# Kernel optimization log

Measured on AMD Instinct MI355X. Metric: run time of the kernel, lower is better.

The kernel has to match this reference:

```python
import jax, jax.numpy as jnp
import numpy as np
from functools import partial

MAX_INSTANCES = 8


def _conv(x, W, b):
    y = jax.lax.conv_general_dilated(x, W, (1, 1), 'SAME',
                                     dimension_numbers=('NHWC', 'HWIO', 'NHWC'))
    return jax.nn.relu(y + b)


def _conv_stack(x, params):
    for W, b in params:
        x = _conv(x, W, b)
    return x


def _resize_and_pad(feat, info, bg_h, bg_w):
    # feat: (h, w, c); info: [y1, y2, x1, x2] fractions of bg size.
    # Bilinear resize (half-pixel centers, like tf.image.resize) of feat to
    # (y_size, x_size), then zero-pad into the (bg_h, bg_w) canvas at
    # (y_front, x_front). Expressed as a fixed-shape gather + validity mask
    # so it is jit-compatible despite data-dependent box sizes.
    h, w, _ = feat.shape
    y_size = jnp.maximum((bg_h * (info[1] - info[0])).astype(jnp.int32), 1)
    x_size = jnp.maximum((bg_w * (info[3] - info[2])).astype(jnp.int32), 1)
    y_front = (bg_h * info[0]).astype(jnp.int32)
    x_front = (bg_w * info[2]).astype(jnp.int32)

    def axis(bg_n, front, size, n_in):
        loc = jnp.arange(bg_n) - front
        valid = (loc >= 0) & (loc < size)
        src = (loc.astype(jnp.float32) + 0.5) * (n_in / size.astype(jnp.float32)) - 0.5
        src = jnp.clip(src, 0.0, n_in - 1.0)
        i0 = jnp.floor(src).astype(jnp.int32)
        i1 = jnp.minimum(i0 + 1, n_in - 1)
        return i0, i1, src - i0.astype(jnp.float32), valid

    y0, y1i, fy, vy = axis(bg_h, y_front, y_size, h)
    x0, x1i, fx, vx = axis(bg_w, x_front, x_size, w)
    g = lambda yi, xi: feat[yi][:, xi]  # (bg_h, bg_w, c)
    fy = fy[:, None, None]
    fx = fx[None, :, None]
    out = (g(y0, x0) * (1 - fy) * (1 - fx) + g(y0, x1i) * (1 - fy) * fx
           + g(y1i, x0) * fy * (1 - fx) + g(y1i, x1i) * fy * fx)
    return out * (vy[:, None] & vx[None, :]).astype(feat.dtype)[:, :, None]


def setup_inputs() -> dict:
    key = jax.random.key(0)
    ks = jax.random.split(key, 16)
    B, H, W, C = 4, 128, 128, 64
    h = w = 64
    hm = wm = 56
    U = 64
    MI = MAX_INSTANCES
    instance_feature = jax.random.normal(ks[0], (B, h, w, C, MI), jnp.float32)
    bg_feature = jax.random.normal(ks[1], (B, H, W, C), jnp.float32)
    # Valid boxes: 0 <= y1 < y2 <= 1, 0 <= x1 < x2 <= 1, layout (B, 4, MI).
    y1 = jax.random.uniform(ks[2], (B, 1, MI), minval=0.0, maxval=0.45)
    hh = jax.random.uniform(ks[3], (B, 1, MI), minval=0.2, maxval=0.5)
    x1 = jax.random.uniform(ks[4], (B, 1, MI), minval=0.0, maxval=0.45)
    ww = jax.random.uniform(ks[5], (B, 1, MI), minval=0.2, maxval=0.5)
    bbox = jnp.concatenate([y1, y1 + hh, x1, x1 + ww], axis=1)
    mrcnn_mask = jax.random.uniform(ks[6], (B, hm, wm, MI), jnp.float32)
    s = 0.05  # small weights keep exp() of relu conv outputs well-scaled
    return {
        'instance_feature': instance_feature,
        'bg_feature': bg_feature,
        'bbox': bbox,
        'mrcnn_mask': mrcnn_mask,
        'iW1': jax.random.normal(ks[7], (3, 3, C, U), jnp.float32) * s,
        'ib1': jnp.zeros((U,), jnp.float32),
        'iW2': jax.random.normal(ks[8], (3, 3, U, U), jnp.float32) * s,
        'ib2': jnp.zeros((U,), jnp.float32),
        'iW3': jax.random.normal(ks[9], (3, 3, U, 1), jnp.float32) * s,
        'ib3': jnp.zeros((1,), jnp.float32),
        'bW1': jax.random.normal(ks[10], (3, 3, C, U), jnp.float32) * s,
        'bb1': jnp.zeros((U,), jnp.float32),
        'bW2': jax.random.normal(ks[11], (3, 3, U, U), jnp.float32) * s,
        'bb2': jnp.zeros((U,), jnp.float32),
        'bW3': jax.random.normal(ks[12], (3, 3, U, 1), jnp.float32) * s,
        'bb3': jnp.zeros((1,), jnp.float32),
    }


def reference(instance_feature, bg_feature, bbox, mrcnn_mask,
              iW1, ib1, iW2, ib2, iW3, ib3,
              bW1, bb1, bW2, bb2, bW3, bb3):
    B, H, W, C = bg_feature.shape
    MI = instance_feature.shape[-1]
    h, w = instance_feature.shape[1], instance_feature.shape[2]
    # pack_instance -> conv stack -> unpack (kept as (B, MI, h, w, 1))
    packed = jnp.transpose(instance_feature, (0, 4, 1, 2, 3)).reshape(B * MI, h, w, C)
    iw = _conv_stack(packed, [(iW1, ib1), (iW2, ib2), (iW3, ib3)]).reshape(B, MI, h, w, 1)
    bgw = _conv_stack(bg_feature, [(bW1, bb1), (bW2, bb2), (bW3, bb3)])  # (B,H,W,1)

    rp = jax.vmap(jax.vmap(partial(_resize_and_pad, bg_h=H, bg_w=W)))
    bbox_t = jnp.transpose(bbox, (0, 2, 1))  # (B, MI, 4)
    rw = rp(iw, bbox_t)  # (B, MI, H, W, 1)
    full = jnp.broadcast_to(jnp.array([0.0, 1.0, 0.0, 1.0], jnp.float32), (B, MI, 4))
    rm = rp(jnp.moveaxis(mrcnn_mask, -1, 1)[..., None], full)  # (B, MI, H, W, 1)
    rsf = rp(jnp.moveaxis(instance_feature, -1, 1), bbox_t)  # (B, MI, H, W, C)

    ew = jnp.exp(rw) * rm          # per-instance exp weight, masked
    ew_bg = jnp.exp(bgw)           # (B, H, W, 1)
    denom = ew.sum(axis=1) + ew_bg  # (B, H, W, 1)
    return (ew_bg / denom) * bg_feature + jnp.sum(rsf * (ew / denom[:, None]), axis=1)
```

## Files before the change

### kernel.cpp

```cpp
#include <hip/hip_runtime.h>
#include <cstdint>

typedef short bf16x8 __attribute__((ext_vector_type(8)));
typedef float f32x4 __attribute__((ext_vector_type(4)));
typedef unsigned short u16;
typedef unsigned short u16x8 __attribute__((ext_vector_type(8)));
typedef unsigned int u32;

__device__ inline u16 f2bf(float f) {
  union { float f; unsigned u; } x; x.f = f;
  unsigned u = x.u + 0x7fffu + ((x.u >> 16) & 1u);
  return (u16)(u >> 16);
}
__device__ inline float bf2f(u16 h) {
  union { unsigned u; float f; } x; x.u = ((unsigned)h) << 16;
  return x.f;
}

__global__ __launch_bounds__(256) void prep_kernel(
    const float* __restrict__ inst, u16* __restrict__ pf,
    const float* __restrict__ w0, const float* __restrict__ w1,
    const float* __restrict__ w2, const float* __restrict__ w3,
    u16* __restrict__ wtr,
    const float* __restrict__ bgf, u16* __restrict__ bgp, int nT)
{
  if ((int)blockIdx.x < nT) {
    const int lane = threadIdx.x & 63;
    const int wvid = blockIdx.x * 4 + (threadIdx.x >> 6);
    const int b = wvid >> 12;
    const int pix = wvid & 4095;
    const float* s = inst + ((size_t)(b * 4096 + pix)) * 512 + lane * 8;
    float4 v0 = *(const float4*)s;
    float4 v1 = *(const float4*)(s + 4);
    float vals[8] = {v0.x, v0.y, v0.z, v0.w, v1.x, v1.y, v1.z, v1.w};
    #pragma unroll
    for (int i = 0; i < 8; i++)
      pf[(((size_t)(b * 8 + i)) * 4096 + pix) * 64 + lane] = f2bf(vals[i]);
  } else if ((int)blockIdx.x < nT + 576) {
    int id = (blockIdx.x - nT) * 256 + threadIdx.x;
    if (id >= 147456) return;
    int s = id / 36864;
    int r = id - s * 36864;
    int tap = r >> 12;
    int rc = r & 4095;
    int c = rc >> 6, u = rc & 63;
    const float* Ws = (s == 0) ? w0 : (s == 1) ? w1 : (s == 2) ? w2 : w3;
    wtr[(size_t)s * 36864 + ((size_t)tap * 64 + u) * 64 + c] =
        f2bf(Ws[((size_t)tap * 64 + c) * 64 + u]);
  } else {
    size_t id = (size_t)(blockIdx.x - nT - 576) * 256 + threadIdx.x;
    const float* s = bgf + id * 8;
    float4 v0 = *(const float4*)s;
    float4 v1 = *(const float4*)(s + 4);
    u16x8 o;
    o[0] = f2bf(v0.x); o[1] = f2bf(v0.y); o[2] = f2bf(v0.z); o[3] = f2bf(v0.w);
    o[4] = f2bf(v1.x); o[5] = f2bf(v1.y); o[6] = f2bf(v1.z); o[7] = f2bf(v1.w);
    *(u16x8*)(bgp + id * 8) = o;
  }
}

#define BOFF 41472
template<int SRC>
__device__ __forceinline__ void conv_body(
    char* smem, const void* __restrict__ inv, const u16* __restrict__ wtr,
    const float* __restrict__ bias, u16* __restrict__ out,
    int H, int W, int bid)
{
  const int tilesX = W >> 4;
  const int tilesPerImg = (H >> 4) * tilesX;
  const int img = bid / tilesPerImg;
  const int tile = bid - img * tilesPerImg;
  const int ty = (tile / tilesX) << 4;
  const int tx = (tile % tilesX) << 4;
  const int tid = threadIdx.x;

  for (int idx = tid; idx < 2592; idx += 256) {
    int hpix = idx >> 3;
    int c0 = (idx & 7) << 3;
    int hy = hpix / 18, hx = hpix - hy * 18;
    int gy = ty + hy - 1, gx = tx + hx - 1;
    u16x8 v = {0, 0, 0, 0, 0, 0, 0, 0};
    if (gy >= 0 && gy < H && gx >= 0 && gx < W) {
      if (SRC == 0) {
        const float* s = (const float*)inv + ((size_t)img * H * W + (size_t)gy * W + gx) * 64 + c0;
        #pragma unroll
        for (int j = 0; j < 8; j++) v[j] = f2bf(s[j]);
      } else if (SRC == 1) {
        const u16* s = (const u16*)inv + ((size_t)img * H * W + (size_t)gy * W + gx) * 64 + c0;
        v = *(const u16x8*)s;
      } else {
        int bb = img >> 3, ii = img & 7;
        const float* s = (const float*)inv + ((((size_t)bb * 64 + gy) * 64 + gx) * 64 + c0) * 8 + ii;
        #pragma unroll
        for (int j = 0; j < 8; j++) v[j] = f2bf(s[j * 8]);
      }
    }
    int byte = (hpix * 128 + c0 * 2) ^ ((hpix & 7) << 4);
    *(u16x8*)(smem + byte) = v;
  }

  const int lane = tid & 63;
  const int wv = tid >> 6;
  const int lrow = lane & 15;
  const int kg = lane >> 4;

  const int ch0 = tid, ch1 = tid + 256;
  const int bu0 = ch0 >> 3, bc0 = (ch0 & 7) << 3;
  const int bu1 = ch1 >> 3, bc1 = (ch1 & 7) << 3;
  const int bdst0 = BOFF + ((bu0 * 128 + bc0 * 2) ^ ((bu0 & 7) << 4));
  const int bdst1 = BOFF + ((bu1 * 128 + bc1 * 2) ^ ((bu1 & 7) << 4));

  {
    u16x8 n0 = *(const u16x8*)(wtr + (size_t)(0 * 64 + bu0) * 64 + bc0);
    u16x8 n1 = *(const u16x8*)(wtr + (size_t)(0 * 64 + bu1) * 64 + bc1);
    *(u16x8*)(smem + bdst0) = n0;
    *(u16x8*)(smem + bdst1) = n1;
  }
  __syncthreads();

  int pyv[4], pxv[4];
  #pragma unroll
  for (int mf = 0; mf < 4; mf++) {
    int p = wv * 64 + mf * 16 + lrow;
    pyv[mf] = p >> 4; pxv[mf] = p & 15;
  }

  f32x4 acc[4][4];
  #pragma unroll
  for (int a = 0; a < 4; a++)
    #pragma unroll
    for (int b = 0; b < 4; b++) { f32x4 z = {0.f, 0.f, 0.f, 0.f}; acc[a][b] = z; }

  for (int tap = 0; tap < 9; tap++) {
    u16x8 n0, n1;
    if (tap < 8) {
      n0 = *(const u16x8*)(wtr + (size_t)((tap + 1) * 64 + bu0) * 64 + bc0);
      n1 = *(const u16x8*)(wtr + (size_t)((tap + 1) * 64 + bu1) * 64 + bc1);
    }
    const int ky = tap / 3, kx = tap - ky * 3;
    #pragma unroll
    for (int ks = 0; ks < 2; ks++) {
      bf16x8 Bf[4];
      #pragma unroll
      for (int nf = 0; nf < 4; nf++) {
        int u = nf * 16 + lrow;
        int byte = BOFF + ((u * 128 + ks * 64 + kg * 16) ^ ((u & 7) << 4));
        Bf[nf] = *(const bf16x8*)(smem + byte);
      }
      #pragma unroll
      for (int mf = 0; mf < 4; mf++) {
        int hpix = (pyv[mf] + ky) * 18 + pxv[mf] + kx;
        int byte = (hpix * 128 + ks * 64 + kg * 16) ^ ((hpix & 7) << 4);
        bf16x8 Af = *(const bf16x8*)(smem + byte);
        #pragma unroll
        for (int nf = 0; nf < 4; nf++)
          acc[mf][nf] = __builtin_amdgcn_mfma_f32_16x16x32_bf16(Af, Bf[nf], acc[mf][nf], 0, 0, 0);
      }
    }
    __syncthreads();
    if (tap < 8) {
      *(u16x8*)(smem + bdst0) = n0;
      *(u16x8*)(smem + bdst1) = n1;
      __syncthreads();
    }
  }

  float bv[4];
  #pragma unroll
  for (int nf = 0; nf < 4; nf++) bv[nf] = bias[nf * 16 + lrow];

  const size_t obase = (size_t)img * H * W;
  #pragma unroll
  for (int mf = 0; mf < 4; mf++) {
    #pragma unroll
    for (int j = 0; j < 4; j++) {
      int p = wv * 64 + mf * 16 + kg * 4 + j;
      int oy = ty + (p >> 4), ox = tx + (p & 15);
      u16* op = out + (obase + (size_t)oy * W + ox) * 64 + lrow;
      #pragma unroll
      for (int nf = 0; nf < 4; nf++)
        op[nf * 16] = f2bf(fmaxf(acc[mf][nf][j] + bv[nf], 0.0f));
    }
  }
}

template<int S1, int S2>
__global__ __launch_bounds__(256) void conv_dual(
    const void* in1, const u16* w1, const float* b1, u16* o1, int H1, int W1, int split,
    const void* in2, const u16* w2, const float* b2, u16* o2, int H2, int W2)
{
  extern __shared__ float4 smem_f4[];
  char* smem = (char*)smem_f4;
  if ((int)blockIdx.x < split)
    conv_body<S1>(smem, in1, w1, b1, o1, H1, W1, blockIdx.x);
  else
    conv_body<S2>(smem, in2, w2, b2, o2, H2, W2, blockIdx.x - split);
}

__device__ __forceinline__ void conv3_body(
    char* smem, const u16* __restrict__ in, const float* __restrict__ W3,
    const float* __restrict__ b3, float* __restrict__ out, int H, int W, int bid)
{
  float* wlds = (float*)(smem + 41472);
  const int tilesX = W >> 4;
  const int tilesPerImg = (H >> 4) * tilesX;
  const int img = bid / tilesPerImg;
  const int tile = bid - img * tilesPerImg;
  const int ty = (tile / tilesX) << 4;
  const int tx = (tile % tilesX) << 4;
  const int tid = threadIdx.x;

  for (int idx = tid; idx < 2592; idx += 256) {
    int hpix = idx >> 3;
    int c0 = (idx & 7) << 3;
    int hy = hpix / 18, hx = hpix - hy * 18;
    int gy = ty + hy - 1, gx = tx + hx - 1;
    u16x8 v = {0, 0, 0, 0, 0, 0, 0, 0};
    if (gy >= 0 && gy < H && gx >= 0 && gx < W)
      v = *(const u16x8*)(in + ((size_t)img * H * W + (size_t)gy * W + gx) * 64 + c0);
    int byte = (hpix * 128 + c0 * 2) ^ ((hpix & 7) << 4);
    *(u16x8*)(smem + byte) = v;
  }
  for (int idx = tid; idx < 576; idx += 256) wlds[idx] = W3[idx];
  __syncthreads();

  const int py = tid >> 4, px = tid & 15;
  float acc = 0.0f;
  #pragma unroll
  for (int ky = 0; ky < 3; ky++) {
    #pragma unroll
    for (int kx = 0; kx < 3; kx++) {
      const int hpix = (py + ky) * 18 + (px + kx);
      const float* wp = wlds + (ky * 3 + kx) * 64;
      #pragma unroll
      for (int cg = 0; cg < 8; cg++) {
        int byte = (hpix * 128 + cg * 16) ^ ((hpix & 7) << 4);
        u16x8 v = *(const u16x8*)(smem + byte);
        #pragma unroll
        for (int j = 0; j < 8; j++)
          acc = fmaf(bf2f(v[j]), wp[cg * 8 + j], acc);
      }
    }
  }
  out[(size_t)img * H * W + (size_t)(ty + py) * W + (tx + px)] =
      fmaxf(acc + b3[0], 0.0f);
}

__global__ __launch_bounds__(256) void conv3_dual(
    const u16* in1, const float* W31, const float* b31, float* o1, int H1, int W1, int split,
    const u16* in2, const float* W32, const float* b32, float* o2, int H2, int W2)
{
  extern __shared__ float4 smem_f4[];
  char* smem = (char*)smem_f4;
  if ((int)blockIdx.x < split)
    conv3_body(smem, in1, W31, b31, o1, H1, W1, blockIdx.x);
  else
    conv3_body(smem, in2, W32, b32, o2, H2, W2, blockIdx.x - split);
}

__global__ __launch_bounds__(256) void precompute_params(
    const float* __restrict__ bbox, const float* __restrict__ mask,
    const float* __restrict__ iw, const float* __restrict__ bgw,
    float* __restrict__ pp_wbg, float4* __restrict__ pp_s)
{
  const int gpix = blockIdx.x * 256 + threadIdx.x;
  const int b = gpix >> 14;
  const int p = gpix & 16383;
  const int Y = p >> 7, X = p & 127;

  float msy = ((float)Y + 0.5f) * 0.4375f - 0.5f;
  msy = fminf(fmaxf(msy, 0.0f), 55.0f);
  int my0 = (int)floorf(msy); int my1 = min(my0 + 1, 55); float fmy = msy - (float)my0;
  float msx = ((float)X + 0.5f) * 0.4375f - 0.5f;
  msx = fminf(fmaxf(msx, 0.0f), 55.0f);
  int mx0 = (int)floorf(msx); int mx1 = min(mx0 + 1, 55); float fmx = msx - (float)mx0;

  const float ewbg = expf(bgw[gpix]);
  float denom = ewbg;
  float wi_l[8];
  u32 yx_l[8];
  float fy_l[8], fx_l[8];

  #pragma unroll
  for (int i = 0; i < 8; i++) {
    float by1 = bbox[(b * 4 + 0) * 8 + i];
    float by2 = bbox[(b * 4 + 1) * 8 + i];
    float bx1 = bbox[(b * 4 + 2) * 8 + i];
    float bx2 = bbox[(b * 4 + 3) * 8 + i];
    int ysz = max((int)(128.0f * (by2 - by1)), 1);
    int xsz = max((int)(128.0f * (bx2 - bx1)), 1);
    int yfr = (int)(128.0f * by1);
    int xfr = (int)(128.0f * bx1);
    int ly = Y - yfr, lx = X - xfr;
    bool valid = (ly >= 0) && (ly < ysz) && (lx >= 0) && (lx < xsz);
    float rwv = 0.0f;
    int y0 = 0, y1i = 0, x0 = 0, x1i = 0;
    float fy = 0.0f, fx = 0.0f;
    if (valid) {
      float sy = ((float)ly + 0.5f) * (64.0f / (float)ysz) - 0.5f;
      sy = fminf(fmaxf(sy, 0.0f), 63.0f);
      y0 = (int)floorf(sy); y1i = min(y0 + 1, 63); fy = sy - (float)y0;
      float sx = ((float)lx + 0.5f) * (64.0f / (float)xsz) - 0.5f;
      sx = fminf(fmaxf(sx, 0.0f), 63.0f);
      x0 = (int)floorf(sx); x1i = min(x0 + 1, 63); fx = sx - (float)x0;
      const float* iwp = iw + ((size_t)(b * 8 + i)) * 4096;
      float v00 = iwp[y0 * 64 + x0],  v01 = iwp[y0 * 64 + x1i];
      float v10 = iwp[y1i * 64 + x0], v11 = iwp[y1i * 64 + x1i];
      rwv = v00 * (1.f - fy) * (1.f - fx) + v01 * (1.f - fy) * fx
          + v10 * fy * (1.f - fx)         + v11 * fy * fx;
    }
    const float* mp = mask + (size_t)b * 56 * 56 * 8 + i;
    float m00 = mp[(my0 * 56 + mx0) * 8], m01 = mp[(my0 * 56 + mx1) * 8];
    float m10 = mp[(my1 * 56 + mx0) * 8], m11 = mp[(my1 * 56 + mx1) * 8];
    float rm = m00 * (1.f - fmy) * (1.f - fmx) + m01 * (1.f - fmy) * fmx
             + m10 * fmy * (1.f - fmx)         + m11 * fmy * fmx;
    float ew = expf(rwv) * rm;
    denom += ew;
    wi_l[i] = valid ? ew : 0.0f;
    yx_l[i] = (u32)y0 | ((u32)x0 << 8) | ((u32)y1i << 16) | ((u32)x1i << 24);
    fy_l[i] = fy; fx_l[i] = fx;
  }

  const float invd = 1.0f / denom;
  pp_wbg[gpix] = ewbg * invd;
  float4* qs = pp_s + ((size_t)gpix << 3);
  #pragma unroll
  for (int i = 0; i < 8; i++) {
    float4 q;
    q.x = wi_l[i] * invd;
    q.y = fy_l[i];
    q.z = fx_l[i];
    q.w = __uint_as_float(yx_l[i]);
    qs[i] = q;
  }
}

__global__ __launch_bounds__(256) void final_blend(
    const u16* __restrict__ pf, const float* __restrict__ bgf,
    const float* __restrict__ pp_wbg, const float4* __restrict__ pp_s,
    float* __restrict__ out)
{
  const int lane = threadIdx.x & 63;
  const int gpix = blockIdx.x * 4 + (threadIdx.x >> 6);
  const int b = gpix >> 14;

  float4 q[8];
  const float4* qs = pp_s + ((size_t)gpix << 3);
  #pragma unroll
  for (int i = 0; i < 8; i++) q[i] = qs[i];

  float accv = pp_wbg[gpix] * bgf[(size_t)gpix * 64 + lane];
  const u16* pfb = pf + (size_t)b * 8 * 262144;
  #pragma unroll
  for (int i = 0; i < 8; i++) {
    if (q[i].x != 0.0f) {
      u32 yx = __float_as_uint(q[i].w);
      int y0 = yx & 255, x0 = (yx >> 8) & 255;
      int y1i = (yx >> 16) & 255, x1i = (yx >> 24) & 255;
      const u16* fp = pfb + (size_t)i * 262144;
      float g00 = bf2f(fp[((size_t)(y0 * 64 + x0)) * 64 + lane]);
      float g01 = bf2f(fp[((size_t)(y0 * 64 + x1i)) * 64 + lane]);
      float g10 = bf2f(fp[((size_t)(y1i * 64 + x0)) * 64 + lane]);
      float g11 = bf2f(fp[((size_t)(y1i * 64 + x1i)) * 64 + lane]);
      float s = g00 * (1.f - q[i].y) * (1.f - q[i].z) + g01 * (1.f - q[i].y) * q[i].z
              + g10 * q[i].y * (1.f - q[i].z)         + g11 * q[i].y * q[i].z;
      accv = fmaf(q[i].x, s, accv);
    }
  }
  out[(size_t)gpix * 64 + lane] = accv;
}

__global__ __launch_bounds__(256) void final_kernel_fb(
    const float* __restrict__ inst, const float* __restrict__ bgf,
    const float* __restrict__ bbox, const float* __restrict__ mask,
    const float* __restrict__ iw, const float* __restrict__ bgw,
    float* __restrict__ out)
{
  const int lane = threadIdx.x & 63;
  const int wvid = blockIdx.x * 4 + (threadIdx.x >> 6);
  const int nw = gridDim.x * 4;
  for (int pix = wvid; pix < 4 * 128 * 128; pix += nw) {
    const int b = pix >> 14;
    const int p = pix & 16383;
    const int Y = p >> 7, X = p & 127;

    float msy = ((float)Y + 0.5f) * 0.4375f - 0.5f;
    msy = fminf(fmaxf(msy, 0.0f), 55.0f);
    int my0 = (int)floorf(msy); int my1 = min(my0 + 1, 55); float fmy = msy - (float)my0;
    float msx = ((float)X + 0.5f) * 0.4375f - 0.5f;
    msx = fminf(fmaxf(msx, 0.0f), 55.0f);
    int mx0 = (int)floorf(msx); int mx1 = min(mx0 + 1, 55); float fmx = msx - (float)mx0;

    const float ewbg = expf(bgw[(size_t)b * 16384 + p]);
    float denom = ewbg;
    float acc = 0.0f;

    for (int i = 0; i < 8; i++) {
      float by1 = bbox[(b * 4 + 0) * 8 + i];
      float by2 = bbox[(b * 4 + 1) * 8 + i];
      float bx1 = bbox[(b * 4 + 2) * 8 + i];
      float bx2 = bbox[(b * 4 + 3) * 8 + i];
      int ysz = max((int)(128.0f * (by2 - by1)), 1);
      int xsz = max((int)(128.0f * (bx2 - bx1)), 1);
      int yfr = (int)(128.0f * by1);
      int xfr = (int)(128.0f * bx1);
      int ly = Y - yfr, lx = X - xfr;
      bool valid = (ly >= 0) && (ly < ysz) && (lx >= 0) && (lx < xsz);
      float rwv = 0.0f;
      int y0 = 0, y1i = 0, x0 = 0, x1i = 0;
      float fy = 0.0f, fx = 0.0f;
      if (valid) {
        float sy = ((float)ly + 0.5f) * (64.0f / (float)ysz) - 0.5f;
        sy = fminf(fmaxf(sy, 0.0f), 63.0f);
        y0 = (int)floorf(sy); y1i = min(y0 + 1, 63); fy = sy - (float)y0;
        float sx = ((float)lx + 0.5f) * (64.0f / (float)xsz) - 0.5f;
        sx = fminf(fmaxf(sx, 0.0f), 63.0f);
        x0 = (int)floorf(sx); x1i = min(x0 + 1, 63); fx = sx - (float)x0;
        const float* iwp = iw + ((size_t)(b * 8 + i)) * 4096;
        float v00 = iwp[y0 * 64 + x0],  v01 = iwp[y0 * 64 + x1i];
        float v10 = iwp[y1i * 64 + x0], v11 = iwp[y1i * 64 + x1i];
        rwv = v00 * (1.f - fy) * (1.f - fx) + v01 * (1.f - fy) * fx
            + v10 * fy * (1.f - fx)         + v11 * fy * fx;
      }
      const float* mp = mask + (size_t)b * 56 * 56 * 8 + i;
      float m00 = mp[(my0 * 56 + mx0) * 8], m01 = mp[(my0 * 56 + mx1) * 8];
      float m10 = mp[(my1 * 56 + mx0) * 8], m11 = mp[(my1 * 56 + mx1) * 8];
      float rm = m00 * (1.f - fmy) * (1.f - fmx) + m01 * (1.f - fmy) * fmx
               + m10 * fmy * (1.f - fmx)         + m11 * fmy * fmx;
      float ew = expf(rwv) * rm;
      denom += ew;
      if (valid) {
        const float* fp = inst + (size_t)b * 2097152 + i;
        float g00 = fp[(((size_t)y0 * 64 + x0) * 64 + lane) * 8];
        float g01 = fp[(((size_t)y0 * 64 + x1i) * 64 + lane) * 8];
        float g10 = fp[(((size_t)y1i * 64 + x0) * 64 + lane) * 8];
        float g11 = fp[(((size_t)y1i * 64 + x1i) * 64 + lane) * 8];
        float s = g00 * (1.f - fy) * (1.f - fx) + g01 * (1.f - fy) * fx
                + g10 * fy * (1.f - fx)         + g11 * fy * fx;
        acc += ew * s;
      }
    }
    const float bgv = bgf[((size_t)b * 16384 + p) * 64 + lane];
    out[((size_t)b * 16384 + p) * 64 + lane] = (ewbg * bgv + acc) / denom;
  }
}

extern "C" void kernel_launch(void* const* d_in, const int* in_sizes, int n_in,
                              void* d_out, int out_size, void* d_ws, size_t ws_size,
                              hipStream_t stream) {
  const float* inst = (const float*)d_in[0];
  const float* bgf  = (const float*)d_in[1];
  const float* bbox = (const float*)d_in[2];
  const float* mask = (const float*)d_in[3];
  const float* iW1 = (const float*)d_in[4];  const float* ib1 = (const float*)d_in[5];
  const float* iW2 = (const float*)d_in[6];  const float* ib2 = (const float*)d_in[7];
  const float* iW3 = (const float*)d_in[8];  const float* ib3 = (const float*)d_in[9];
  const float* bW1 = (const float*)d_in[10]; const float* bb1 = (const float*)d_in[11];
  const float* bW2 = (const float*)d_in[12]; const float* bb2 = (const float*)d_in[13];
  const float* bW3 = (const float*)d_in[14]; const float* bb3 = (const float*)d_in[15];

  char* ws = (char*)d_ws;
  u16*   wtr  = (u16*)ws;
  u16*   AbI  = (u16*)(ws + 294912);
  u16*   AbB  = (u16*)(ws + 17072128);
  u16*   BbI  = (u16*)(ws + 25460736);
  u16*   BbB  = (u16*)(ws + 42237952);
  float* iw   = (float*)(ws + 50626560);
  float* bgw  = (float*)(ws + 51150848);
  u16*   pf   = (u16*)(ws + 51412992);
  u16*   bgp  = (u16*)(ws + 68190208);
  const bool usePf = ws_size >= (size_t)76578816;
  float* outp = (float*)d_out;

  float*  pp_wbg = (float*) (ws + 294912);
  float4* pp_s   = (float4*)(ws + 294912 + 262144);

  if (usePf) {
    prep_kernel<<<6720, 256, 0, stream>>>(inst, pf, iW1, iW2, bW1, bW2, wtr,
                                          bgf, bgp, 4096);
    conv_dual<1, 1><<<768, 256, 49664, stream>>>(
        pf,  wtr,             ib1, AbI, 64, 64, 512,
        bgp, wtr + 2 * 36864, bb1, AbB, 128, 128);
    conv_dual<1, 1><<<768, 256, 49664, stream>>>(
        AbI, wtr + 36864,     ib2, BbI, 64, 64, 512,
        AbB, wtr + 3 * 36864, bb2, BbB, 128, 128);
    conv3_dual<<<768, 256, 43776, stream>>>(
        BbI, iW3, ib3, iw, 64, 64, 512,
        BbB, bW3, bb3, bgw, 128, 128);
    precompute_params<<<256, 256, 0, stream>>>(bbox, mask, iw, bgw, pp_wbg, pp_s);
    final_blend<<<16384, 256, 0, stream>>>(pf, bgf, pp_wbg, pp_s, outp);
  } else {
    prep_kernel<<<576, 256, 0, stream>>>(inst, pf, iW1, iW2, bW1, bW2, wtr,
                                         bgf, bgp, 0);
    conv_dual<2, 0><<<768, 256, 49664, stream>>>(
        inst, wtr,            ib1, AbI, 64, 64, 512,
        bgf, wtr + 2 * 36864, bb1, AbB, 128, 128);
    conv_dual<1, 1><<<768, 256, 49664, stream>>>(
        AbI, wtr + 36864,     ib2, BbI, 64, 64, 512,
        AbB, wtr + 3 * 36864, bb2, BbB, 128, 128);
    conv3_dual<<<768, 256, 43776, stream>>>(
        BbI, iW3, ib3, iw, 64, 64, 512,
        BbB, bW3, bb3, bgw, 128, 128);
    final_kernel_fb<<<2048, 256, 0, stream>>>(inst, bgf, bbox, mask, iw, bgw, outp);
  }
}
```

Before: 115.1 us.

## Enlarge conv tiles to 32x16 and double-buffer weight slices in LDS

The 3x3 conv kernels now process 32x16 output tiles per block, with 8 M-fragments per wave, so the halo overhead per output and the number of blocks both shrink. Weight tap slices are double-buffered in LDS, which removes one __syncthreads per tap. Shared memory is now statically sized (about 93KB), and launch bounds are set to one block per CU. The cost is fewer blocks (384) and higher register pressure from 32 accumulators per lane, which may reduce occupancy and latency hiding.

```diff
diff --git a/kernel.cpp b/kernel.cpp
--- a/kernel.cpp
+++ b/kernel.cpp
@@ -59,7 +59,7 @@
   }
 }
 
-#define BOFF 41472
+#define BOFF0 78336
 template<int SRC>
 __device__ __forceinline__ void conv_body(
     char* smem, const void* __restrict__ inv, const u16* __restrict__ wtr,
@@ -67,14 +67,14 @@
     int H, int W, int bid)
 {
   const int tilesX = W >> 4;
-  const int tilesPerImg = (H >> 4) * tilesX;
+  const int tilesPerImg = (H >> 5) * tilesX;
   const int img = bid / tilesPerImg;
   const int tile = bid - img * tilesPerImg;
-  const int ty = (tile / tilesX) << 4;
+  const int ty = (tile / tilesX) << 5;
   const int tx = (tile % tilesX) << 4;
   const int tid = threadIdx.x;
 
-  for (int idx = tid; idx < 2592; idx += 256) {
+  for (int idx = tid; idx < 4896; idx += 256) {
     int hpix = idx >> 3;
     int c0 = (idx & 7) << 3;
     int hy = hpix / 18, hx = hpix - hy * 18;
@@ -107,27 +107,27 @@
   const int ch0 = tid, ch1 = tid + 256;
   const int bu0 = ch0 >> 3, bc0 = (ch0 & 7) << 3;
   const int bu1 = ch1 >> 3, bc1 = (ch1 & 7) << 3;
-  const int bdst0 = BOFF + ((bu0 * 128 + bc0 * 2) ^ ((bu0 & 7) << 4));
-  const int bdst1 = BOFF + ((bu1 * 128 + bc1 * 2) ^ ((bu1 & 7) << 4));
+  const int brel0 = (bu0 * 128 + bc0 * 2) ^ ((bu0 & 7) << 4);
+  const int brel1 = (bu1 * 128 + bc1 * 2) ^ ((bu1 & 7) << 4);
 
   {
-    u16x8 n0 = *(const u16x8*)(wtr + (size_t)(0 * 64 + bu0) * 64 + bc0);
-    u16x8 n1 = *(const u16x8*)(wtr + (size_t)(0 * 64 + bu1) * 64 + bc1);
-    *(u16x8*)(smem + bdst0) = n0;
-    *(u16x8*)(smem + bdst1) = n1;
+    u16x8 n0 = *(const u16x8*)(wtr + (size_t)bu0 * 64 + bc0);
+    u16x8 n1 = *(const u16x8*)(wtr + (size_t)bu1 * 64 + bc1);
+    *(u16x8*)(smem + BOFF0 + brel0) = n0;
+    *(u16x8*)(smem + BOFF0 + brel1) = n1;
   }
   __syncthreads();
 
-  int pyv[4], pxv[4];
-  #pragma unroll
-  for (int mf = 0; mf < 4; mf++) {
-    int p = wv * 64 + mf * 16 + lrow;
+  int pyv[8], pxv[8];
+  #pragma unroll
+  for (int mf = 0; mf < 8; mf++) {
+    int p = wv * 128 + mf * 16 + lrow;
     pyv[mf] = p >> 4; pxv[mf] = p & 15;
   }
 
-  f32x4 acc[4][4];
-  #pragma unroll
-  for (int a = 0; a < 4; a++)
+  f32x4 acc[8][4];
+  #pragma unroll
+  for (int a = 0; a < 8; a++)
     #pragma unroll
     for (int b = 0; b < 4; b++) { f32x4 z = {0.f, 0.f, 0.f, 0.f}; acc[a][b] = z; }
 
@@ -138,17 +138,18 @@
       n1 = *(const u16x8*)(wtr + (size_t)((tap + 1) * 64 + bu1) * 64 + bc1);
     }
     const int ky = tap / 3, kx = tap - ky * 3;
+    const int bbase = BOFF0 + ((tap & 1) << 13);
     #pragma unroll
     for (int ks = 0; ks < 2; ks++) {
       bf16x8 Bf[4];
       #pragma unroll
       for (int nf = 0; nf < 4; nf++) {
         int u = nf * 16 + lrow;
-        int byte = BOFF + ((u * 128 + ks * 64 + kg * 16) ^ ((u & 7) << 4));
+        int byte = bbase + ((u * 128 + ks * 64 + kg * 16) ^ ((u & 7) << 4));
         Bf[nf] = *(const bf16x8*)(smem + byte);
       }
       #pragma unroll
-      for (int mf = 0; mf < 4; mf++) {
+      for (int mf = 0; mf < 8; mf++) {
         int hpix = (pyv[mf] + ky) * 18 + pxv[mf] + kx;
         int byte = (hpix * 128 + ks * 64 + kg * 16) ^ ((hpix & 7) << 4);
         bf16x8 Af = *(const bf16x8*)(smem + byte);
@@ -157,10 +158,10 @@
           acc[mf][nf] = __builtin_amdgcn_mfma_f32_16x16x32_bf16(Af, Bf[nf], acc[mf][nf], 0, 0, 0);
       }
     }
-    __syncthreads();
     if (tap < 8) {
-      *(u16x8*)(smem + bdst0) = n0;
-      *(u16x8*)(smem + bdst1) = n1;
+      const int nb = BOFF0 + (((tap + 1) & 1) << 13);
+      *(u16x8*)(smem + nb + brel0) = n0;
+      *(u16x8*)(smem + nb + brel1) = n1;
       __syncthreads();
     }
   }
@@ -171,10 +172,10 @@
 
   const size_t obase = (size_t)img * H * W;
   #pragma unroll
-  for (int mf = 0; mf < 4; mf++) {
+  for (int mf = 0; mf < 8; mf++) {
     #pragma unroll
     for (int j = 0; j < 4; j++) {
-      int p = wv * 64 + mf * 16 + kg * 4 + j;
+      int p = wv * 128 + mf * 16 + kg * 4 + j;
       int oy = ty + (p >> 4), ox = tx + (p & 15);
       u16* op = out + (obase + (size_t)oy * W + ox) * 64 + lrow;
       #pragma unroll
@@ -185,12 +186,11 @@
 }
 
 template<int S1, int S2>
-__global__ __launch_bounds__(256) void conv_dual(
+__global__ __launch_bounds__(256, 1) void conv_dual(
     const void* in1, const u16* w1, const float* b1, u16* o1, int H1, int W1, int split,
     const void* in2, const u16* w2, const float* b2, u16* o2, int H2, int W2)
 {
-  extern __shared__ float4 smem_f4[];
-  char* smem = (char*)smem_f4;
+  __shared__ __align__(16) char smem[94720];
   if ((int)blockIdx.x < split)
     conv_body<S1>(smem, in1, w1, b1, o1, H1, W1, blockIdx.x);
   else
@@ -250,8 +250,7 @@
     const u16* in1, const float* W31, const float* b31, float* o1, int H1, int W1, int split,
     const u16* in2, const float* W32, const float* b32, float* o2, int H2, int W2)
 {
-  extern __shared__ float4 smem_f4[];
-  char* smem = (char*)smem_f4;
+  __shared__ __align__(16) char smem[43776];
   if ((int)blockIdx.x < split)
     conv3_body(smem, in1, W31, b31, o1, H1, W1, blockIdx.x);
   else
@@ -478,13 +477,13 @@
   if (usePf) {
     prep_kernel<<<6720, 256, 0, stream>>>(inst, pf, iW1, iW2, bW1, bW2, wtr,
                                           bgf, bgp, 4096);
-    conv_dual<1, 1><<<768, 256, 49664, stream>>>(
-        pf,  wtr,             ib1, AbI, 64, 64, 512,
+    conv_dual<1, 1><<<384, 256, 0, stream>>>(
+        pf,  wtr,             ib1, AbI, 64, 64, 256,
         bgp, wtr + 2 * 36864, bb1, AbB, 128, 128);
-    conv_dual<1, 1><<<768, 256, 49664, stream>>>(
-        AbI, wtr + 36864,     ib2, BbI, 64, 64, 512,
+    conv_dual<1, 1><<<384, 256, 0, stream>>>(
+        AbI, wtr + 36864,     ib2, BbI, 64, 64, 256,
         AbB, wtr + 3 * 36864, bb2, BbB, 128, 128);
-    conv3_dual<<<768, 256, 43776, stream>>>(
+    conv3_dual<<<768, 256, 0, stream>>>(
         BbI, iW3, ib3, iw, 64, 64, 512,
         BbB, bW3, bb3, bgw, 128, 128);
     precompute_params<<<256, 256, 0, stream>>>(bbox, mask, iw, bgw, pp_wbg, pp_s);
@@ -492,13 +491,13 @@
   } else {
     prep_kernel<<<576, 256, 0, stream>>>(inst, pf, iW1, iW2, bW1, bW2, wtr,
                                          bgf, bgp, 0);
-    conv_dual<2, 0><<<768, 256, 49664, stream>>>(
-        inst, wtr,            ib1, AbI, 64, 64, 512,
+    conv_dual<2, 0><<<384, 256, 0, stream>>>(
+        inst, wtr,            ib1, AbI, 64, 64, 256,
         bgf, wtr + 2 * 36864, bb1, AbB, 128, 128);
-    conv_dual<1, 1><<<768, 256, 49664, stream>>>(
-        AbI, wtr + 36864,     ib2, BbI, 64, 64, 512,
+    conv_dual<1, 1><<<384, 256, 0, stream>>>(
+        AbI, wtr + 36864,     ib2, BbI, 64, 64, 256,
         AbB, wtr + 3 * 36864, bb2, BbB, 128, 128);
-    conv3_dual<<<768, 256, 43776, stream>>>(
+    conv3_dual<<<768, 256, 0, stream>>>(
         BbI, iW3, ib3, iw, 64, 64, 512,
         BbB, bW3, bb3, bgw, 128, 128);
     final_kernel_fb<<<2048, 256, 0, stream>>>(inst, bgf, bbox, mask, iw, bgw, outp);
```

Result: slower. 155.6 us (+35.2%).
